# Kernel optimization log

Measured on AMD Instinct MI355X. Metric: run time of the kernel, lower is better.

## Reference

```python
import jax, jax.numpy as jnp
import numpy as np

B, G, D_EMB = 4096, 20000, 512
H_LOW, N_HIDDEN = 512, 1024
TOPK, T, FILM_W = 64, 0.1, 1.0
LN_EPS = 1e-5


def _layer_norm(x, gamma, beta):
    mu = jnp.mean(x, axis=-1, keepdims=True)
    var = jnp.mean(jnp.square(x - mu), axis=-1, keepdims=True)
    return (x - mu) * jax.lax.rsqrt(var + LN_EPS) * gamma + beta


def _l2norm(x, eps=1e-12):
    n = jnp.sqrt(jnp.sum(jnp.square(x), axis=-1, keepdims=True))
    return x / jnp.maximum(n, eps)


def setup_inputs() -> dict:
    key = jax.random.key(0)
    ks = jax.random.split(key, 8)
    s = 0.02
    return {
        "x": jax.random.normal(ks[0], (B, G), jnp.float32),
        "g": jax.random.normal(ks[1], (G, D_EMB), jnp.float32),
        "W_enc": jax.random.normal(ks[2], (H_LOW, G), jnp.float32) * s,
        "b_enc": jnp.zeros((H_LOW,), jnp.float32),
        "ln1_g": jnp.ones((H_LOW,), jnp.float32),
        "ln1_b": jnp.zeros((H_LOW,), jnp.float32),
        "W_ga": jax.random.normal(ks[3], (H_LOW, D_EMB), jnp.float32) * s,
        "W_gamma": jax.random.normal(ks[4], (H_LOW, H_LOW), jnp.float32) * s,
        "b_gamma": jnp.zeros((H_LOW,), jnp.float32),
        "W_beta": jax.random.normal(ks[5], (H_LOW, H_LOW), jnp.float32) * s,
        "b_beta": jnp.zeros((H_LOW,), jnp.float32),
        "W_exp": jax.random.normal(ks[6], (N_HIDDEN, H_LOW), jnp.float32) * s,
        "b_exp": jnp.zeros((N_HIDDEN,), jnp.float32),
        "ln2_g": jnp.ones((N_HIDDEN,), jnp.float32),
        "ln2_b": jnp.zeros((N_HIDDEN,), jnp.float32),
    }


def reference(x, g, W_enc, b_enc, ln1_g, ln1_b, W_ga, W_gamma, b_gamma,
              W_beta, b_beta, W_exp, b_exp, ln2_g, ln2_b):
    # x_encoder: Linear -> LayerNorm -> GELU (dropout = eval no-op)
    h = jnp.dot(x, W_enc.T) + b_enc                    # [B, H_LOW]
    h = jax.nn.gelu(_layer_norm(h, ln1_g, ln1_b), approximate=False)
    # gene adapter + cosine scores
    e = _l2norm(jnp.dot(g, W_ga.T))                    # [G, H_LOW]
    h_x = _l2norm(h)                                   # [B, H_LOW]
    scores = jnp.dot(h_x, e.T) / T                     # [B, G]
    # top-k mask + masked softmax attention
    _, idx = jax.lax.top_k(scores, TOPK)               # [B, TOPK]
    mask = jnp.zeros_like(scores).at[jnp.arange(B)[:, None], idx].set(1.0)
    attn = jax.nn.softmax(jnp.where(mask == 0, -1e9, scores), axis=-1)
    ctx = jnp.dot(attn, e)                             # [B, H_LOW]
    # FiLM (identity-centered)
    gamma = (jnp.dot(ctx, W_gamma.T) + b_gamma) * FILM_W
    beta = (jnp.dot(ctx, W_beta.T) + b_beta) * FILM_W
    h_cell = (1.0 + gamma) * h_x + beta
    # x_expand: Linear -> LayerNorm -> GELU
    h2 = jnp.dot(h_cell, W_exp.T) + b_exp              # [B, N_HIDDEN]
    return jax.nn.gelu(_layer_norm(h2, ln2_g, ln2_b), approximate=False)
```

## Files before the change

### kernel.cpp

```cpp
#include <hip/hip_runtime.h>
#include <hip/hip_fp16.h>
#include <math.h>
#include <type_traits>

#define DEVI __device__ __forceinline__

typedef __attribute__((ext_vector_type(8))) short bf16x8;
typedef __attribute__((ext_vector_type(4))) float f32x4;
typedef __attribute__((ext_vector_type(4))) unsigned int u32x4;
typedef unsigned short ushort_t;

DEVI unsigned int pack_bf16(float a, float b) {
  unsigned int ua = __float_as_uint(a), ub = __float_as_uint(b);
  ua = (ua + 0x7FFFu + ((ua >> 16) & 1u)) >> 16;
  ub = (ub + 0x7FFFu + ((ub >> 16) & 1u)) >> 16;
  return ua | (ub << 16);
}

DEVI bf16x8 cvt_bf16x8(f32x4 lo, f32x4 hi) {
  unsigned int r0, r1, r2, r3;
  asm("v_cvt_pk_bf16_f32 %0, %1, %2" : "=v"(r0) : "v"(lo[0]), "v"(lo[1]));
  asm("v_cvt_pk_bf16_f32 %0, %1, %2" : "=v"(r1) : "v"(lo[2]), "v"(lo[3]));
  asm("v_cvt_pk_bf16_f32 %0, %1, %2" : "=v"(r2) : "v"(hi[0]), "v"(hi[1]));
  asm("v_cvt_pk_bf16_f32 %0, %1, %2" : "=v"(r3) : "v"(hi[2]), "v"(hi[3]));
  union { u32x4 u; bf16x8 v; } x;
  x.u = u32x4{r0, r1, r2, r3};
  return x.v;
}

template<int SPLITZ, typename OutT>
__global__ __launch_bounds__(512, 1) void bgemm256(
    const ushort_t* __restrict__ A, const ushort_t* __restrict__ B,
    OutT* __restrict__ C, int M, int N, int K, int nbn, int nbm)
{
  __shared__ __align__(16) char L[131072];
  const int tid = threadIdx.x, lane = tid & 63, wv = tid >> 6;

  const int nwg = gridDim.x;
  const int hw = blockIdx.x;
  const int q = nwg >> 3, r = nwg & 7;
  const int xcd = hw & 7, pos = hw >> 3;
  const int lid = (xcd < r ? xcd * (q + 1) : r * (q + 1) + (xcd - r) * q) + pos;
  const int bn = lid % nbn;
  const int t2 = lid / nbn;
  const int bm = t2 % nbm;
  const int z  = t2 / nbm;

  const int ksteps = K >> 6;
  int kbBeg = 0, kbEnd = ksteps;
  if (SPLITZ > 1) {
    const int sz = (ksteps + SPLITZ - 1) / SPLITZ;
    kbBeg = z * sz;
    kbEnd = min(ksteps, kbBeg + sz);
  }

  const int wm = wv >> 2, wn = wv & 3;
  const int lrow = lane & 15, kg = lane >> 4;

  f32x4 acc[8][4];
#pragma unroll
  for (int i = 0; i < 8; ++i)
#pragma unroll
    for (int j = 0; j < 4; ++j) acc[i][j] = f32x4{0.f, 0.f, 0.f, 0.f};

  const int sr = lane >> 2, sq = lane & 3;
  const ushort_t* aS[2];
  const ushort_t* bS[2];
#pragma unroll
  for (int j = 0; j < 2; ++j) {
    const int lr = (wv * 2 + j) * 16 + sr;
    const int swz = (lr ^ (lr >> 2)) & 3;
    aS[j] = A + (size_t)min(bm * 256 + lr, M - 1) * (size_t)K + ((sq ^ swz) << 3);
    bS[j] = B + (size_t)min(bn * 256 + lr, N - 1) * (size_t)K + ((sq ^ swz) << 3);
  }

  int offA[8], offB[4];
#pragma unroll
  for (int i = 0; i < 8; ++i) {
    const int ra = wm * 128 + i * 16 + lrow;
    offA[i] = ra * 64 + (((kg ^ ((ra ^ (ra >> 2)) & 3))) << 4);
  }
#pragma unroll
  for (int j = 0; j < 4; ++j) {
    const int rb = wn * 64 + j * 16 + lrow;
    offB[j] = rb * 64 + (((kg ^ ((rb ^ (rb >> 2)) & 3))) << 4);
  }

#define G256_STG(isB, h, k0v) do {                                            \
    _Pragma("unroll")                                                         \
    for (int j_ = 0; j_ < 2; ++j_)                                            \
      __builtin_amdgcn_global_load_lds(                                       \
          (const __attribute__((address_space(1))) void*)                     \
              (((isB) ? bS : aS)[j_] + (k0v) + (h) * 32),                     \
          (__attribute__((address_space(3))) void*)                           \
              (L + (isB) * 65536 + (s ^ 1) * 32768 + (h) * 16384 +            \
               (wv * 2 + j_) * 1024), 16, 0, 0);                              \
  } while (0)
#define G256_RDA(h, rg) do {                                                  \
    _Pragma("unroll")                                                         \
    for (int i_ = 0; i_ < 4; ++i_)                                            \
      af[i_] = *(const bf16x8*)(L + s * 32768 + (h) * 16384 +                 \
                                offA[(rg) * 4 + i_]);                         \
  } while (0)
#define G256_RDB(h) do {                                                      \
    _Pragma("unroll")                                                         \
    for (int j_ = 0; j_ < 4; ++j_)                                            \
      bfv[j_] = *(const bf16x8*)(L + 65536 + s * 32768 + (h) * 16384 +        \
                                 offB[j_]);                                   \
  } while (0)
#define G256_MM(rg) do {                                                      \
    _Pragma("unroll")                                                         \
    for (int i_ = 0; i_ < 4; ++i_)                                            \
      _Pragma("unroll")                                                       \
      for (int j_ = 0; j_ < 4; ++j_)                                          \
        acc[(rg) * 4 + i_][j_] = __builtin_amdgcn_mfma_f32_16x16x32_bf16(     \
            af[i_], bfv[j_], acc[(rg) * 4 + i_][j_], 0, 0, 0);                \
  } while (0)
#define G256_BAR asm volatile("s_barrier" ::: "memory")

  {
    int s = 1;
    const int k0 = kbBeg << 6;
    G256_STG(0, 0, k0);
    G256_STG(1, 0, k0);
    G256_STG(0, 1, k0);
    G256_STG(1, 1, k0);
  }
  asm volatile("s_waitcnt vmcnt(4)" ::: "memory");
  G256_BAR;

  int s = 0;
  for (int t = kbBeg; t < kbEnd; ++t) {
    const bool more = (t + 1 < kbEnd);
    const int k0n = (t + 1) << 6;
    bf16x8 af[4], bfv[4];
    G256_RDB(0);
    G256_RDA(0, 0);
    if (more) G256_STG(0, 0, k0n);
    G256_BAR;
    __builtin_amdgcn_s_setprio(1);
    G256_MM(0);
    __builtin_amdgcn_s_setprio(0);
    G256_BAR;
    G256_RDA(0, 1);
    if (more) G256_STG(1, 0, k0n);
    G256_BAR;
    __builtin_amdgcn_s_setprio(1);
    G256_MM(1);
    __builtin_amdgcn_s_setprio(0);
    if (more) asm volatile("s_waitcnt vmcnt(4)" ::: "memory");
    else      asm volatile("s_waitcnt vmcnt(0)" ::: "memory");
    G256_BAR;
    G256_RDB(1);
    G256_RDA(1, 0);
    if (more) G256_STG(0, 1, k0n);
    G256_BAR;
    __builtin_amdgcn_s_setprio(1);
    G256_MM(0);
    __builtin_amdgcn_s_setprio(0);
    G256_BAR;
    G256_RDA(1, 1);
    if (more) G256_STG(1, 1, k0n);
    G256_BAR;
    __builtin_amdgcn_s_setprio(1);
    G256_MM(1);
    __builtin_amdgcn_s_setprio(0);
    if (more) asm volatile("s_waitcnt vmcnt(4)" ::: "memory");
    G256_BAR;
    s ^= 1;
  }
#undef G256_STG
#undef G256_RDA
#undef G256_RDB
#undef G256_MM
#undef G256_BAR

  const size_t zoff = (SPLITZ > 1) ? (size_t)z * (size_t)M * (size_t)N : 0;
#pragma unroll
  for (int i = 0; i < 8; ++i) {
#pragma unroll
    for (int j = 0; j < 4; ++j) {
      const int col = bn * 256 + wn * 64 + j * 16 + lrow;
      if (col >= N) continue;
      const int row0 = bm * 256 + wm * 128 + i * 16 + kg * 4;
#pragma unroll
      for (int rr = 0; rr < 4; ++rr) {
        const int gr = row0 + rr;
        if (gr < M) {
          const float v = acc[i][j][rr];
          if constexpr (std::is_same<OutT, __half>::value)
            C[zoff + (size_t)gr * (size_t)N + col] = __float2half(v);
          else
            C[zoff + (size_t)gr * (size_t)N + col] = v;
        }
      }
    }
  }
}

template<typename AT, int SPLITZ, bool DUALB, bool BIAS, typename OutT>
__global__ __launch_bounds__(512, sizeof(AT) == 2 ? 3 : 2) void bgemm(
    const AT* __restrict__ A, const ushort_t* __restrict__ B0,
    const ushort_t* __restrict__ B1, const float* __restrict__ bias0,
    const float* __restrict__ bias1, OutT* __restrict__ C,
    int M, int N, int K, int nbn, int nbm)
{
  constexpr bool AB16 = (sizeof(AT) == 2);
  __shared__ __align__(16) char AsB[AB16 ? 16384 : 32768];
  __shared__ __align__(16) char BsB[32768];
  const int tid = threadIdx.x, lane = tid & 63, wv = tid >> 6;

  const int nwg = gridDim.x;
  const int hw = blockIdx.x;
  const int q = nwg >> 3, r = nwg & 7;
  const int xcd = hw & 7, pos = hw >> 3;
  const int lid = (xcd < r ? xcd * (q + 1) : r * (q + 1) + (xcd - r) * q) + pos;
  const int bn = lid % nbn;
  const int t2 = lid / nbn;
  const int bm = t2 % nbm;
  const int z  = t2 / nbm;

  const ushort_t* B  = (DUALB && z == 1) ? B1 : B0;
  const float* bias  = (DUALB && z == 1) ? bias1 : bias0;

  const int ksteps = (K + 63) >> 6;
  int kbBeg = 0, kbEnd = ksteps;
  if (SPLITZ > 1) {
    const int sz = (ksteps + SPLITZ - 1) / SPLITZ;
    kbBeg = z * sz;
    kbEnd = min(ksteps, kbBeg + sz);
  }

  const int wr = (wv >> 2) * 64;
  const int wc = (wv & 3) * 64;
  const int lrow = lane & 15, kg = lane >> 4;

  f32x4 acc[4][4];
#pragma unroll
  for (int i = 0; i < 4; ++i)
#pragma unroll
    for (int j = 0; j < 4; ++j) acc[i][j] = f32x4{0.f, 0.f, 0.f, 0.f};

  const AT* aSrc[4];
  if constexpr (AB16) {
    const int r0 = lane >> 3;
    const int ce = ((lane & 7) ^ r0) << 3;
#pragma unroll
    for (int j = 0; j < 2; ++j) {
      const int row = wv * 16 + j * 8 + r0;
      aSrc[j] = A + (size_t)min(bm * 128 + row, M - 1) * (size_t)K + ce;
    }
  } else {
    const int r0 = lane >> 4;
#pragma unroll
    for (int j = 0; j < 4; ++j) {
      const int row = wv * 16 + j * 4 + r0;
      const int ca = ((lane & 15) << 2) ^ ((row & 7) << 3);
      aSrc[j] = A + (size_t)min(bm * 128 + row, M - 1) * (size_t)K + ca;
    }
  }
  const int rB0 = lane >> 3;
  const int colB = ((lane & 7) ^ rB0) << 3;
  const ushort_t* bSrc[4];
#pragma unroll
  for (int j = 0; j < 4; ++j) {
    const int row = wv * 32 + j * 8 + rB0;
    bSrc[j] = B + (size_t)min(bn * 256 + row, N - 1) * (size_t)K + colB;
  }

  for (int kb = kbBeg; kb < kbEnd; ++kb) {
    const int k0 = kb << 6;
    if constexpr (AB16) {
#pragma unroll
      for (int j = 0; j < 2; ++j)
        __builtin_amdgcn_global_load_lds(
            (const __attribute__((address_space(1))) void*)(aSrc[j] + k0),
            (__attribute__((address_space(3))) void*)(AsB + (wv * 2 + j) * 1024),
            16, 0, 0);
    } else {
#pragma unroll
      for (int j = 0; j < 4; ++j)
        __builtin_amdgcn_global_load_lds(
            (const __attribute__((address_space(1))) void*)(aSrc[j] + k0),
            (__attribute__((address_space(3))) void*)(AsB + (wv * 4 + j) * 1024),
            16, 0, 0);
    }
#pragma unroll
    for (int j = 0; j < 4; ++j)
      __builtin_amdgcn_global_load_lds(
          (const __attribute__((address_space(1))) void*)(bSrc[j] + k0),
          (__attribute__((address_space(3))) void*)(BsB + (wv * 4 + j) * 1024),
          16, 0, 0);
    __syncthreads();
#pragma unroll
    for (int kk = 0; kk < 2; ++kk) {
      bf16x8 af[4], bfr[4];
#pragma unroll
      for (int i = 0; i < 4; ++i) {
        const int ra = wr + i * 16 + lrow;
        if constexpr (AB16) {
          af[i] = *(const bf16x8*)(AsB + ra * 128 + ((((kk << 2) + kg) ^ (ra & 7)) << 4));
        } else {
          const char* pa = AsB + ra * 256 + ((kk * 128 + (kg << 5)) ^ ((ra & 7) << 5));
          af[i] = cvt_bf16x8(*(const f32x4*)pa, *(const f32x4*)(pa + 16));
        }
        const int rb = wc + i * 16 + lrow;
        bfr[i] = *(const bf16x8*)(BsB + rb * 128 + ((((kk << 2) + kg) ^ (rb & 7)) << 4));
      }
#pragma unroll
      for (int i = 0; i < 4; ++i)
#pragma unroll
        for (int j = 0; j < 4; ++j)
          acc[i][j] = __builtin_amdgcn_mfma_f32_16x16x32_bf16(af[i], bfr[j], acc[i][j], 0, 0, 0);
    }
    __syncthreads();
  }

  const size_t zoff = (SPLITZ > 1 || DUALB) ? (size_t)z * (size_t)M * (size_t)N : 0;
#pragma unroll
  for (int i = 0; i < 4; ++i) {
#pragma unroll
    for (int j = 0; j < 4; ++j) {
      const int col = bn * 256 + wc + j * 16 + lrow;
      if (col >= N) continue;
      const int row0 = bm * 128 + wr + i * 16 + kg * 4;
      float bv = 0.f;
      if (BIAS) bv = bias[col];
#pragma unroll
      for (int rr = 0; rr < 4; ++rr) {
        const int gr = row0 + rr;
        if (gr < M) {
          const float v = acc[i][j][rr] + bv;
          if constexpr (std::is_same<OutT, __half>::value)
            C[zoff + (size_t)gr * (size_t)N + col] = __float2half(v);
          else
            C[zoff + (size_t)gr * (size_t)N + col] = v;
        }
      }
    }
  }
}

__global__ __launch_bounds__(256) void f2b(
    const float4* __restrict__ in, u32x4* __restrict__ out, int n8)
{
  const int i = blockIdx.x * 256 + threadIdx.x;
  if (i < n8) {
    const float4 a = in[2 * i], b = in[2 * i + 1];
    u32x4 o = { pack_bf16(a.x, a.y), pack_bf16(a.z, a.w),
                pack_bf16(b.x, b.y), pack_bf16(b.z, b.w) };
    out[i] = o;
  }
}

template<int K0_8, int KP_8>
__global__ __launch_bounds__(256) void f2b_pad(
    const float* __restrict__ in, u32x4* __restrict__ out, int total)
{
  const int i = blockIdx.x * 256 + threadIdx.x;
  if (i >= total) return;
  const int row = i / KP_8, c8 = i % KP_8;
  u32x4 o = {0u, 0u, 0u, 0u};
  if (c8 < K0_8) {
    const float4* p = (const float4*)(in + (size_t)row * (K0_8 * 8) + c8 * 8);
    const float4 a = p[0], b = p[1];
    o = u32x4{ pack_bf16(a.x, a.y), pack_bf16(a.z, a.w),
               pack_bf16(b.x, b.y), pack_bf16(b.z, b.w) };
  }
  out[i] = o;
}

__global__ __launch_bounds__(256) void gee_fuse_ln1(
    const float* __restrict__ P, const float* __restrict__ b_enc,
    const float* __restrict__ g1, const float* __restrict__ b1,
    float* __restrict__ hx, unsigned int* __restrict__ hxb)
{
  const int row = blockIdx.x, tid = threadIdx.x;
  __shared__ float red[16];
  const size_t MN = (size_t)4096 * 512;
  const size_t o2 = (size_t)row * 256 + tid;
  float2 v = ((const float2*)b_enc)[tid];
#pragma unroll
  for (int qq = 0; qq < 8; ++qq) {
    const float2 p = ((const float2*)P)[qq * (MN / 2) + o2];
    v.x += p.x; v.y += p.y;
  }
  float a = v.x + v.y;
  float b = v.x * v.x + v.y * v.y;
#pragma unroll
  for (int o = 32; o > 0; o >>= 1) { a += __shfl_xor(a, o); b += __shfl_xor(b, o); }
  const int lane = tid & 63, wvi = tid >> 6;
  if (lane == 0) { red[wvi] = a; red[8 + wvi] = b; }
  __syncthreads();
  const float mu  = (red[0] + red[1] + red[2] + red[3]) * (1.f / 512.f);
  const float ex2 = (red[8] + red[9] + red[10] + red[11]) * (1.f / 512.f);
  const float inv = rsqrtf(ex2 - mu * mu + 1e-5f);
  const float2 gg = ((const float2*)g1)[tid];
  const float2 bb = ((const float2*)b1)[tid];
  const float y0 = (v.x - mu) * inv * gg.x + bb.x;
  const float y1 = (v.y - mu) * inv * gg.y + bb.y;
  const float t0 = 0.5f * y0 * (1.f + erff(y0 * 0.70710678118654752f));
  const float t1 = 0.5f * y1 * (1.f + erff(y1 * 0.70710678118654752f));
  float ss = t0 * t0 + t1 * t1;
  __syncthreads();
#pragma unroll
  for (int o = 32; o > 0; o >>= 1) ss += __shfl_xor(ss, o);
  if (lane == 0) red[wvi] = ss;
  __syncthreads();
  const float sc = 1.f / fmaxf(sqrtf(red[0] + red[1] + red[2] + red[3]), 1e-12f);
  const float h0 = t0 * sc, h1 = t1 * sc;
  ((float2*)hx)[o2] = make_float2(h0, h1);
  hxb[o2] = pack_bf16(h0, h1);
}

__global__ __launch_bounds__(256) void gee_l2rows(
    const __half2* __restrict__ ein, unsigned int* __restrict__ eb)
{
  const int row = blockIdx.x, tid = threadIdx.x;
  __shared__ float red[4];
  const __half2 h = ein[(size_t)row * 256 + tid];
  const float vx = __half2float(h.x), vy = __half2float(h.y);
  float ss = vx * vx + vy * vy;
#pragma unroll
  for (int o = 32; o > 0; o >>= 1) ss += __shfl_xor(ss, o);
  if ((tid & 63) == 0) red[tid >> 6] = ss;
  __syncthreads();
  const float sc = 1.f / fmaxf(sqrtf(red[0] + red[1] + red[2] + red[3]), 1e-12f);
  eb[(size_t)row * 256 + tid] = pack_bf16(vx * sc, vy * sc);
}

__global__ __launch_bounds__(256) void gee_topk(
    const __half* __restrict__ scores, int* __restrict__ oidx, float* __restrict__ ow)
{
  constexpr int G = 20000, GP = G / 2, CAP = 2048, TCAP = 160;
  const int row = blockIdx.x, tid = threadIdx.x;
  const int lane = tid & 63, wv = tid >> 6;
  __shared__ int hist[4][256];
  __shared__ int cnt_ge[256];
  __shared__ int wtop[4];
  __shared__ unsigned int comp[CAP];
  __shared__ int whist[4][16];
  __shared__ int sel[64];
  __shared__ int tie[TCAP];
  __shared__ int s_thr, s_above, s_cand, s_cnt, s_n1, s_n2;

  const unsigned int* srow32 =
      (const unsigned int*)((const ushort_t*)scores + (size_t)row * G);
  const ushort_t* srow16 = (const ushort_t*)srow32;

#pragma unroll
  for (int b = 0; b < 4; ++b) hist[b][tid] = 0;
  if (tid == 0) { s_cnt = 0; s_n1 = 0; s_n2 = 0; }
  __syncthreads();

  for (int j0 = 0; j0 < GP; j0 += 256) {
    const int j = j0 + tid;
    if (j < GP) {
      const unsigned int p = srow32[j];
      const unsigned int f = (((p >> 15) & 0x10001u) * 0x7FFFu) + 0x80008000u;
      const unsigned int k2 = p ^ f;
      atomicAdd(&hist[wv][(k2 >> 8) & 0xFFu], 1);
      atomicAdd(&hist[wv][k2 >> 24], 1);
    }
  }
  __syncthreads();
  cnt_ge[tid] = hist[0][tid] + hist[1][tid] + hist[2][tid] + hist[3][tid];
  __syncthreads();
  for (int off = 1; off < 256; off <<= 1) {
    const int add = (tid + off < 256) ? cnt_ge[tid + off] : 0;
    __syncthreads();
    cnt_ge[tid] += add;
    __syncthreads();
  }
  {
    const unsigned long long m = __ballot(cnt_ge[tid] >= 64);
    if (lane == 0) wtop[wv] = m ? (wv * 64 + 63 - __clzll(m)) : -1;
  }
  __syncthreads();
  if (tid == 0) {
    const int thrB = max(max(wtop[0], wtop[1]), max(wtop[2], wtop[3]));
    s_cand  = cnt_ge[thrB];
    s_above = (thrB == 255) ? 0 : cnt_ge[thrB + 1];
    s_thr   = thrB << 8;
  }
  __syncthreads();

  const bool useComp = (s_cand <= CAP);
  const unsigned int thrB = ((unsigned int)s_thr) >> 8;

  if (useComp) {
    for (int j0 = 0; j0 < GP; j0 += 256) {
      const int j = j0 + tid;
      if (j < GP) {
        const unsigned int p = srow32[j];
        const unsigned int f = (((p >> 15) & 0x10001u) * 0x7FFFu) + 0x80008000u;
        const unsigned int k2 = p ^ f;
        const unsigned int lo = k2 & 0xFFFFu, hi = k2 >> 16;
        if ((lo >> 8) >= thrB) {
          const int pos = atomicAdd(&s_cnt, 1);
          comp[pos] = (lo << 16) | (unsigned)(2 * j);
        }
        if ((hi >> 8) >= thrB) {
          const int pos = atomicAdd(&s_cnt, 1);
          comp[pos] = (hi << 16) | (unsigned)(2 * j + 1);
        }
      }
    }
  }
  __syncthreads();
  const int Nloop = useComp ? s_cnt : G;

  for (int pass = 2; pass < 4; ++pass) {
    const int shift = 12 - 4 * pass;
    const unsigned int thr = (unsigned int)s_thr;
    const unsigned int pfx = thr >> (shift + 4);
    int c[16];
#pragma unroll
    for (int b = 0; b < 16; ++b) c[b] = 0;
    for (int j0 = 0; j0 < Nloop; j0 += 256) {
      const int j = j0 + tid;
      const bool ok = j < Nloop;
      unsigned int key;
      if (useComp) {
        key = ok ? (comp[j] >> 16) : 0u;
      } else {
        const unsigned int raw = ok ? (unsigned int)srow16[j] : 0u;
        key = (raw & 0x8000u) ? (0xFFFFu & ~raw) : (raw | 0x8000u);
      }
      const unsigned int nb = (ok && (key >> (shift + 4)) == pfx) ? ((key >> shift) & 15u) : 0xFFu;
#pragma unroll
      for (int b = 0; b < 16; ++b) c[b] += __popcll(__ballot(nb == (unsigned)b));
    }
    if (lane == 0) {
#pragma unroll
      for (int b = 0; b < 16; ++b) whist[wv][b] = c[b];
    }
    __syncthreads();
    if (tid == 0) {
      int run = s_above;
      for (int vv = 15; vv >= 0; --vv) {
        const int c4 = whist[0][vv] + whist[1][vv] + whist[2][vv] + whist[3][vv];
        if (run + c4 >= 64) { s_thr |= vv << shift; break; }
        run += c4;
      }
      s_above = run;
    }
    __syncthreads();
  }

  const unsigned int kthr = (unsigned int)s_thr;
  for (int j0 = 0; j0 < Nloop; j0 += 256) {
    const int j = j0 + tid;
    if (j < Nloop) {
      unsigned int key, idx;
      if (useComp) {
        const unsigned int u = comp[j];
        key = u >> 16; idx = u & 0xFFFFu;
      } else {
        const unsigned int raw = (unsigned int)srow16[j];
        key = (raw & 0x8000u) ? (0xFFFFu & ~raw) : (raw | 0x8000u);
        idx = (unsigned)j;
      }
      if (key > kthr) {
        const int pos = atomicAdd(&s_n1, 1);
        sel[pos] = (int)idx;
      } else if (key == kthr) {
        const int pos = atomicAdd(&s_n2, 1);
        if (pos < TCAP) tie[pos] = (int)idx;
      }
    }
  }
  __syncthreads();
  if (tid == 0) {
    const int n1 = s_n1;
    const int n2 = min(s_n2, TCAP);
    const int need = 64 - n1;
    for (int rr = 0; rr < need; ++rr) {
      int best = 1 << 30, bj = 0;
      for (int j = 0; j < n2; ++j)
        if (tie[j] < best) { best = tie[j]; bj = j; }
      sel[n1 + rr] = best;
      tie[bj] = 1 << 30;
    }
  }
  __syncthreads();
  if (tid < 64) {
    const int idx = sel[tid];
    const float sv = __half2float(scores[(size_t)row * G + idx]) * 10.0f;
    float m = sv;
#pragma unroll
    for (int o = 32; o > 0; o >>= 1) m = fmaxf(m, __shfl_xor(m, o));
    const float w = __expf(sv - m);
    float d = w;
#pragma unroll
    for (int o = 32; o > 0; o >>= 1) d += __shfl_xor(d, o);
    oidx[(size_t)row * 64 + tid] = idx;
    ow[(size_t)row * 64 + tid] = w / d;
  }
}

__global__ __launch_bounds__(256) void gee_ctx(
    const int* __restrict__ idx, const float* __restrict__ w,
    const unsigned int* __restrict__ eb, unsigned int* __restrict__ ctxb)
{
  const int row = blockIdx.x, tid = threadIdx.x;
  __shared__ int sidx[64];
  __shared__ float sw[64];
  if (tid < 64) { sidx[tid] = idx[(size_t)row * 64 + tid]; sw[tid] = w[(size_t)row * 64 + tid]; }
  __syncthreads();
  float a0 = 0.f, a1 = 0.f;
#pragma unroll 4
  for (int k = 0; k < 64; ++k) {
    const unsigned int pk = eb[(size_t)sidx[k] * 256 + tid];
    const float wk = sw[k];
    a0 += wk * __uint_as_float(pk << 16);
    a1 += wk * __uint_as_float(pk & 0xFFFF0000u);
  }
  ctxb[(size_t)row * 256 + tid] = pack_bf16(a0, a1);
}

__global__ __launch_bounds__(256) void gee_film(
    const float2* __restrict__ gm, const float2* __restrict__ bt,
    const float2* __restrict__ hx, unsigned int* __restrict__ hcb, int n2)
{
  const int i = blockIdx.x * 256 + threadIdx.x;
  if (i < n2) {
    const float2 g = gm[i], b = bt[i], h = hx[i];
    hcb[i] = pack_bf16((1.f + g.x) * h.x + b.x, (1.f + g.y) * h.y + b.y);
  }
}

__global__ __launch_bounds__(256) void gee_ln2(
    const float* __restrict__ h2, const float* __restrict__ g2,
    const float* __restrict__ b2, float* __restrict__ out)
{
  const int row = blockIdx.x, tid = threadIdx.x;
  __shared__ float red[16];
  float v[4];
  float a = 0.f, b = 0.f;
#pragma unroll
  for (int e = 0; e < 4; ++e) {
    v[e] = h2[(size_t)row * 1024 + tid + e * 256];
    a += v[e]; b += v[e] * v[e];
  }
#pragma unroll
  for (int o = 32; o > 0; o >>= 1) { a += __shfl_xor(a, o); b += __shfl_xor(b, o); }
  const int lane = tid & 63, wvi = tid >> 6;
  if (lane == 0) { red[wvi] = a; red[8 + wvi] = b; }
  __syncthreads();
  const float mu  = (red[0] + red[1] + red[2] + red[3]) * (1.f / 1024.f);
  const float ex2 = (red[8] + red[9] + red[10] + red[11]) * (1.f / 1024.f);
  const float inv = rsqrtf(ex2 - mu * mu + 1e-5f);
#pragma unroll
  for (int e = 0; e < 4; ++e) {
    const int c = tid + e * 256;
    const float y = (v[e] - mu) * inv * g2[c] + b2[c];
    out[(size_t)row * 1024 + c] = 0.5f * y * (1.f + erff(y * 0.70710678118654752f));
  }
}

extern "C" void kernel_launch(void* const* d_in, const int* in_sizes, int n_in,
                              void* d_out, int out_size, void* d_ws, size_t ws_size,
                              hipStream_t stream)
{
  const float* x       = (const float*)d_in[0];
  const float* g       = (const float*)d_in[1];
  const float* W_enc   = (const float*)d_in[2];
  const float* b_enc   = (const float*)d_in[3];
  const float* ln1_g   = (const float*)d_in[4];
  const float* ln1_b   = (const float*)d_in[5];
  const float* W_ga    = (const float*)d_in[6];
  const float* W_gamma = (const float*)d_in[7];
  const float* b_gamma = (const float*)d_in[8];
  const float* W_beta  = (const float*)d_in[9];
  const float* b_beta  = (const float*)d_in[10];
  const float* W_exp   = (const float*)d_in[11];
  const float* b_exp   = (const float*)d_in[12];
  const float* ln2_g   = (const float*)d_in[13];
  const float* ln2_b   = (const float*)d_in[14];
  float* out = (float*)d_out;

  char* ws = (char*)d_ws;
  constexpr size_t OFF_XB     = 0;
  constexpr size_t OFF_SCORES = 0;
  constexpr size_t OFF_GA     = 0;
  constexpr size_t OFF_BE     = 8388608;
  constexpr size_t OFF_H2     = 16777216;
  constexpr size_t OFF_PART   = 164626432;
  constexpr size_t OFF_WENCB  = 231735296;
  constexpr size_t OFF_E      = 231735296;
  constexpr size_t OFF_EB     = 252313600;
  constexpr size_t OFF_HX     = 272793600;
  constexpr size_t OFF_HXB    = 281182208;
  constexpr size_t OFF_CTXB   = 285376512;
  constexpr size_t OFF_HCB    = 289570816;
  constexpr size_t OFF_WGAB   = 293765120;
  constexpr size_t OFF_WGMB   = 294289408;
  constexpr size_t OFF_WBTB   = 294813696;
  constexpr size_t OFF_WEXB   = 295337984;
  constexpr size_t OFF_TIDX   = 296386560;
  constexpr size_t OFF_TW     = 297435136;

  ushort_t*     xb     = (ushort_t*)(ws + OFF_XB);
  __half*       scores = (__half*)(ws + OFF_SCORES);
  float*        ga     = (float*)(ws + OFF_GA);
  float*        be     = (float*)(ws + OFF_BE);
  float*        h2     = (float*)(ws + OFF_H2);
  float*        part   = (float*)(ws + OFF_PART);
  ushort_t*     wencb  = (ushort_t*)(ws + OFF_WENCB);
  __half*       e      = (__half*)(ws + OFF_E);
  unsigned int* eb     = (unsigned int*)(ws + OFF_EB);
  float*        hx     = (float*)(ws + OFF_HX);
  unsigned int* hxb    = (unsigned int*)(ws + OFF_HXB);
  unsigned int* ctxb   = (unsigned int*)(ws + OFF_CTXB);
  unsigned int* hcb    = (unsigned int*)(ws + OFF_HCB);
  ushort_t*     wgab   = (ushort_t*)(ws + OFF_WGAB);
  ushort_t*     wgmb   = (ushort_t*)(ws + OFF_WGMB);
  ushort_t*     wbtb   = (ushort_t*)(ws + OFF_WBTB);
  ushort_t*     wexb   = (ushort_t*)(ws + OFF_WEXB);
  int*          tidx   = (int*)(ws + OFF_TIDX);
  float*        tw     = (float*)(ws + OFF_TW);

  f2b_pad<2500, 2512><<<40192, 256, 0, stream>>>(x, (u32x4*)xb, 4096 * 2512);
  f2b_pad<2500, 2512><<<5024, 256, 0, stream>>>(W_enc, (u32x4*)wencb, 512 * 2512);
  f2b<<<128, 256, 0, stream>>>((const float4*)W_ga,    (u32x4*)wgab, 32768);
  f2b<<<128, 256, 0, stream>>>((const float4*)W_gamma, (u32x4*)wgmb, 32768);
  f2b<<<128, 256, 0, stream>>>((const float4*)W_beta,  (u32x4*)wbtb, 32768);
  f2b<<<256, 256, 0, stream>>>((const float4*)W_exp,   (u32x4*)wexb, 65536);

  bgemm256<8, float><<<256, 512, 0, stream>>>(
      xb, wencb, part, 4096, 512, 20096, 2, 16);
  gee_fuse_ln1<<<4096, 256, 0, stream>>>(part, b_enc, ln1_g, ln1_b, hx, hxb);
  bgemm<float, 1, false, false, __half><<<314, 512, 0, stream>>>(
      g, wgab, nullptr, nullptr, nullptr, e, 20000, 512, 512, 2, 157);
  gee_l2rows<<<20000, 256, 0, stream>>>((const __half2*)e, eb);
  bgemm256<1, __half><<<1264, 512, 0, stream>>>(
      (const ushort_t*)hxb, (const ushort_t*)eb, scores, 4096, 20000, 512, 79, 16);
  gee_topk<<<4096, 256, 0, stream>>>(scores, tidx, tw);
  gee_ctx<<<4096, 256, 0, stream>>>(tidx, tw, eb, ctxb);
  bgemm<ushort_t, 1, true, true, float><<<128, 512, 0, stream>>>(
      (const ushort_t*)ctxb, wgmb, wbtb, b_gamma, b_beta, ga, 4096, 512, 512, 2, 32);
  gee_film<<<4096, 256, 0, stream>>>((const float2*)ga, (const float2*)be,
                                     (const float2*)hx, hcb, 1048576);
  bgemm<ushort_t, 1, false, true, float><<<128, 512, 0, stream>>>(
      (const ushort_t*)hcb, wexb, nullptr, b_exp, nullptr, h2, 4096, 1024, 512, 4, 32);
  gee_ln2<<<4096, 256, 0, stream>>>(h2, ln2_g, ln2_b, out);
}
```

Baseline: 561.5 us.

## Read fp32 x directly in encoder GEMM and fuse top-k with context gather

The explicit fp32-to-bf16 padded conversion of x (4096x20000) is replaced by a new GEMM that streams fp32 A tiles into LDS and converts them to bf16 in registers before the MFMA. This drops a full extra read and write of the large input, at the cost of doubled LDS/global traffic per A tile, a 128-row tile and a split-K of 4, plus a scalar tail for the unpadded K. Separately, the top-k kernel now performs the weighted context gather itself, which removes the index/weight round trip through global memory and one kernel launch.

```diff
diff --git a/kernel.cpp b/kernel.cpp
--- a/kernel.cpp
+++ b/kernel.cpp
@@ -26,6 +26,187 @@
   union { u32x4 u; bf16x8 v; } x;
   x.u = u32x4{r0, r1, r2, r3};
   return x.v;
+}
+
+template<int SPLITZ, bool TAIL>
+__global__ __launch_bounds__(512, 1) void bgemmA32(
+    const float* __restrict__ A, const ushort_t* __restrict__ B,
+    float* __restrict__ C, int M, int N, int K, int nbn, int nbm)
+{
+  __shared__ __align__(16) char L[131072];
+  const int tid = threadIdx.x, lane = tid & 63, wv = tid >> 6;
+
+  const int nwg = gridDim.x;
+  const int hw = blockIdx.x;
+  const int q = nwg >> 3, r = nwg & 7;
+  const int xcd = hw & 7, pos = hw >> 3;
+  const int lid = (xcd < r ? xcd * (q + 1) : r * (q + 1) + (xcd - r) * q) + pos;
+  const int bn = lid % nbn;
+  const int t2 = lid / nbn;
+  const int bm = t2 % nbm;
+  const int z  = t2 / nbm;
+
+  const int ksteps = K >> 6;
+  const int szk = (ksteps + SPLITZ - 1) / SPLITZ;
+  const int kbBeg = z * szk;
+  const int kbEnd = min(ksteps, kbBeg + szk);
+
+  const int wm = wv >> 2, wn = wv & 3;
+  const int lrow = lane & 15, kg = lane >> 4;
+
+  f32x4 acc[4][4];
+#pragma unroll
+  for (int i = 0; i < 4; ++i)
+#pragma unroll
+    for (int j = 0; j < 4; ++j) acc[i][j] = f32x4{0.f, 0.f, 0.f, 0.f};
+
+  const int alr = lane >> 3, ag32 = (lane & 7) >> 1;
+  const float* aS[2];
+#pragma unroll
+  for (int j = 0; j < 2; ++j) {
+    const int lr = (wv * 2 + j) * 8 + alr;
+    const int swz = (lr ^ (lr >> 2)) & 3;
+    const int colf = ((ag32 ^ swz) << 3) + (lane & 1) * 4;
+    aS[j] = A + (size_t)min(bm * 128 + lr, M - 1) * (size_t)K + colf;
+  }
+  const int blr = lane >> 2, bgq = lane & 3;
+  const ushort_t* bS[2];
+#pragma unroll
+  for (int j = 0; j < 2; ++j) {
+    const int lr = (wv * 2 + j) * 16 + blr;
+    const int swz = (lr ^ (lr >> 2)) & 3;
+    aS[j] = aS[j];
+    bS[j] = B + (size_t)min(bn * 256 + lr, N - 1) * (size_t)K + ((bgq ^ swz) << 3);
+  }
+
+  int offA[4], offB[4];
+#pragma unroll
+  for (int i = 0; i < 4; ++i) {
+    const int ra = wm * 64 + i * 16 + lrow;
+    offA[i] = ra * 128 + ((kg ^ ((ra ^ (ra >> 2)) & 3)) << 5);
+  }
+#pragma unroll
+  for (int j = 0; j < 4; ++j) {
+    const int rb = wn * 64 + j * 16 + lrow;
+    offB[j] = rb * 64 + ((kg ^ ((rb ^ (rb >> 2)) & 3)) << 4);
+  }
+
+#define GA_STGA(h, k0v) do {                                                  \
+    _Pragma("unroll")                                                         \
+    for (int j_ = 0; j_ < 2; ++j_)                                            \
+      __builtin_amdgcn_global_load_lds(                                       \
+          (const __attribute__((address_space(1))) void*)(aS[j_] + (k0v) + (h) * 32), \
+          (__attribute__((address_space(3))) void*)                           \
+              (L + (s ^ 1) * 32768 + (h) * 16384 + (wv * 2 + j_) * 1024),     \
+          16, 0, 0);                                                          \
+  } while (0)
+#define GA_STGB(h, k0v) do {                                                  \
+    _Pragma("unroll")                                                         \
+    for (int j_ = 0; j_ < 2; ++j_)                                            \
+      __builtin_amdgcn_global_load_lds(                                       \
+          (const __attribute__((address_space(1))) void*)(bS[j_] + (k0v) + (h) * 32), \
+          (__attribute__((address_space(3))) void*)                           \
+              (L + 65536 + (s ^ 1) * 32768 + (h) * 16384 + (wv * 2 + j_) * 1024), \
+          16, 0, 0);                                                          \
+  } while (0)
+#define GA_RDB(h) do {                                                        \
+    _Pragma("unroll")                                                         \
+    for (int j_ = 0; j_ < 4; ++j_)                                            \
+      bfv[j_] = *(const bf16x8*)(L + 65536 + s * 32768 + (h) * 16384 + offB[j_]); \
+  } while (0)
+#define GA_RDA(h, rg) do {                                                    \
+    _Pragma("unroll")                                                         \
+    for (int i_ = 0; i_ < 2; ++i_) {                                          \
+      const char* pa_ = L + s * 32768 + (h) * 16384 + offA[(rg) * 2 + i_];    \
+      af[i_] = cvt_bf16x8(*(const f32x4*)pa_, *(const f32x4*)(pa_ + 16));     \
+    }                                                                         \
+  } while (0)
+#define GA_MM(rg) do {                                                        \
+    _Pragma("unroll")                                                         \
+    for (int i_ = 0; i_ < 2; ++i_)                                            \
+      _Pragma("unroll")                                                       \
+      for (int j_ = 0; j_ < 4; ++j_)                                          \
+        acc[(rg) * 2 + i_][j_] = __builtin_amdgcn_mfma_f32_16x16x32_bf16(     \
+            af[i_], bfv[j_], acc[(rg) * 2 + i_][j_], 0, 0, 0);                \
+  } while (0)
+#define GA_BAR asm volatile("s_barrier" ::: "memory")
+
+  {
+    int s = 1;
+    const int k0 = kbBeg << 6;
+    GA_STGA(0, k0); GA_STGB(0, k0); GA_STGA(1, k0); GA_STGB(1, k0);
+  }
+  asm volatile("s_waitcnt vmcnt(4)" ::: "memory");
+  GA_BAR;
+
+  int s = 0;
+  for (int t = kbBeg; t < kbEnd; ++t) {
+    const bool more = (t + 1 < kbEnd);
+    const int k0n = (t + 1) << 6;
+    bf16x8 af[2], bfv[4];
+    GA_RDB(0); GA_RDA(0, 0);
+    if (more) GA_STGA(0, k0n);
+    GA_BAR;
+    __builtin_amdgcn_s_setprio(1); GA_MM(0); __builtin_amdgcn_s_setprio(0);
+    GA_BAR;
+    GA_RDA(0, 1);
+    if (more) GA_STGB(0, k0n);
+    GA_BAR;
+    __builtin_amdgcn_s_setprio(1); GA_MM(1); __builtin_amdgcn_s_setprio(0);
+    if (more) asm volatile("s_waitcnt vmcnt(4)" ::: "memory");
+    else      asm volatile("s_waitcnt vmcnt(0)" ::: "memory");
+    GA_BAR;
+    GA_RDB(1); GA_RDA(1, 0);
+    if (more) GA_STGA(1, k0n);
+    GA_BAR;
+    __builtin_amdgcn_s_setprio(1); GA_MM(0); __builtin_amdgcn_s_setprio(0);
+    GA_BAR;
+    GA_RDA(1, 1);
+    if (more) GA_STGB(1, k0n);
+    GA_BAR;
+    __builtin_amdgcn_s_setprio(1); GA_MM(1); __builtin_amdgcn_s_setprio(0);
+    if (more) asm volatile("s_waitcnt vmcnt(4)" ::: "memory");
+    GA_BAR;
+    s ^= 1;
+  }
+
+  if (TAIL && z == SPLITZ - 1 && (K & 63)) {
+    const int k0t = ksteps << 6;
+    bf16x8 af[2], bfv[4];
+#pragma unroll
+    for (int j = 0; j < 2; ++j) {
+      const float4 av = *(const float4*)(aS[j] + k0t);
+      *(float4*)(L + s * 32768 + (wv * 2 + j) * 1024 + lane * 16) = av;
+      const u32x4 bv = *(const u32x4*)(bS[j] + k0t);
+      *(u32x4*)(L + 65536 + s * 32768 + (wv * 2 + j) * 1024 + lane * 16) = bv;
+    }
+    __syncthreads();
+    GA_RDB(0);
+    GA_RDA(0, 0); GA_MM(0);
+    GA_RDA(0, 1); GA_MM(1);
+  }
+#undef GA_STGA
+#undef GA_STGB
+#undef GA_RDB
+#undef GA_RDA
+#undef GA_MM
+#undef GA_BAR
+
+  const size_t zoff = (SPLITZ > 1) ? (size_t)z * (size_t)M * (size_t)N : 0;
+#pragma unroll
+  for (int i = 0; i < 4; ++i) {
+#pragma unroll
+    for (int j = 0; j < 4; ++j) {
+      const int col = bn * 256 + wn * 64 + j * 16 + lrow;
+      if (col >= N) continue;
+      const int row0 = bm * 128 + wm * 64 + i * 16 + kg * 4;
+#pragma unroll
+      for (int rr = 0; rr < 4; ++rr) {
+        const int gr = row0 + rr;
+        if (gr < M) C[zoff + (size_t)gr * (size_t)N + col] = acc[i][j][rr];
+      }
+    }
+  }
 }
 
 template<int SPLITZ, typename OutT>
@@ -138,16 +319,12 @@
     G256_RDA(0, 0);
     if (more) G256_STG(0, 0, k0n);
     G256_BAR;
-    __builtin_amdgcn_s_setprio(1);
-    G256_MM(0);
-    __builtin_amdgcn_s_setprio(0);
+    __builtin_amdgcn_s_setprio(1); G256_MM(0); __builtin_amdgcn_s_setprio(0);
     G256_BAR;
     G256_RDA(0, 1);
     if (more) G256_STG(1, 0, k0n);
     G256_BAR;
-    __builtin_amdgcn_s_setprio(1);
-    G256_MM(1);
-    __builtin_amdgcn_s_setprio(0);
+    __builtin_amdgcn_s_setprio(1); G256_MM(1); __builtin_amdgcn_s_setprio(0);
     if (more) asm volatile("s_waitcnt vmcnt(4)" ::: "memory");
     else      asm volatile("s_waitcnt vmcnt(0)" ::: "memory");
     G256_BAR;
@@ -155,16 +332,12 @@
     G256_RDA(1, 0);
     if (more) G256_STG(0, 1, k0n);
     G256_BAR;
-    __builtin_amdgcn_s_setprio(1);
-    G256_MM(0);
-    __builtin_amdgcn_s_setprio(0);
+    __builtin_amdgcn_s_setprio(1); G256_MM(0); __builtin_amdgcn_s_setprio(0);
     G256_BAR;
     G256_RDA(1, 1);
     if (more) G256_STG(1, 1, k0n);
     G256_BAR;
-    __builtin_amdgcn_s_setprio(1);
-    G256_MM(1);
-    __builtin_amdgcn_s_setprio(0);
+    __builtin_amdgcn_s_setprio(1); G256_MM(1); __builtin_amdgcn_s_setprio(0);
     if (more) asm volatile("s_waitcnt vmcnt(4)" ::: "memory");
     G256_BAR;
     s ^= 1;
@@ -353,23 +526,6 @@
   }
 }
 
-template<int K0_8, int KP_8>
-__global__ __launch_bounds__(256) void f2b_pad(
-    const float* __restrict__ in, u32x4* __restrict__ out, int total)
-{
-  const int i = blockIdx.x * 256 + threadIdx.x;
-  if (i >= total) return;
-  const int row = i / KP_8, c8 = i % KP_8;
-  u32x4 o = {0u, 0u, 0u, 0u};
-  if (c8 < K0_8) {
-    const float4* p = (const float4*)(in + (size_t)row * (K0_8 * 8) + c8 * 8);
-    const float4 a = p[0], b = p[1];
-    o = u32x4{ pack_bf16(a.x, a.y), pack_bf16(a.z, a.w),
-               pack_bf16(b.x, b.y), pack_bf16(b.z, b.w) };
-  }
-  out[i] = o;
-}
-
 __global__ __launch_bounds__(256) void gee_fuse_ln1(
     const float* __restrict__ P, const float* __restrict__ b_enc,
     const float* __restrict__ g1, const float* __restrict__ b1,
@@ -381,7 +537,7 @@
   const size_t o2 = (size_t)row * 256 + tid;
   float2 v = ((const float2*)b_enc)[tid];
 #pragma unroll
-  for (int qq = 0; qq < 8; ++qq) {
+  for (int qq = 0; qq < 4; ++qq) {
     const float2 p = ((const float2*)P)[qq * (MN / 2) + o2];
     v.x += p.x; v.y += p.y;
   }
@@ -429,8 +585,9 @@
   eb[(size_t)row * 256 + tid] = pack_bf16(vx * sc, vy * sc);
 }
 
-__global__ __launch_bounds__(256) void gee_topk(
-    const __half* __restrict__ scores, int* __restrict__ oidx, float* __restrict__ ow)
+__global__ __launch_bounds__(256) void gee_topk_ctx(
+    const __half* __restrict__ scores, const unsigned int* __restrict__ eb,
+    unsigned int* __restrict__ ctxb)
 {
   constexpr int G = 20000, GP = G / 2, CAP = 2048, TCAP = 160;
   const int row = blockIdx.x, tid = threadIdx.x;
@@ -441,6 +598,7 @@
   __shared__ unsigned int comp[CAP];
   __shared__ int whist[4][16];
   __shared__ int sel[64];
+  __shared__ float swt[64];
   __shared__ int tie[TCAP];
   __shared__ int s_thr, s_above, s_cand, s_cnt, s_n1, s_n2;
 
@@ -594,25 +752,14 @@
     float d = w;
 #pragma unroll
     for (int o = 32; o > 0; o >>= 1) d += __shfl_xor(d, o);
-    oidx[(size_t)row * 64 + tid] = idx;
-    ow[(size_t)row * 64 + tid] = w / d;
-  }
-}
-
-__global__ __launch_bounds__(256) void gee_ctx(
-    const int* __restrict__ idx, const float* __restrict__ w,
-    const unsigned int* __restrict__ eb, unsigned int* __restrict__ ctxb)
-{
-  const int row = blockIdx.x, tid = threadIdx.x;
-  __shared__ int sidx[64];
-  __shared__ float sw[64];
-  if (tid < 64) { sidx[tid] = idx[(size_t)row * 64 + tid]; sw[tid] = w[(size_t)row * 64 + tid]; }
+    swt[tid] = w / d;
+  }
   __syncthreads();
   float a0 = 0.f, a1 = 0.f;
 #pragma unroll 4
   for (int k = 0; k < 64; ++k) {
-    const unsigned int pk = eb[(size_t)sidx[k] * 256 + tid];
-    const float wk = sw[k];
+    const unsigned int pk = eb[(size_t)sel[k] * 256 + tid];
+    const float wk = swt[k];
     a0 += wk * __uint_as_float(pk << 16);
     a1 += wk * __uint_as_float(pk & 0xFFFF0000u);
   }
@@ -681,27 +828,23 @@
   float* out = (float*)d_out;
 
   char* ws = (char*)d_ws;
-  constexpr size_t OFF_XB     = 0;
   constexpr size_t OFF_SCORES = 0;
   constexpr size_t OFF_GA     = 0;
   constexpr size_t OFF_BE     = 8388608;
   constexpr size_t OFF_H2     = 16777216;
-  constexpr size_t OFF_PART   = 164626432;
-  constexpr size_t OFF_WENCB  = 231735296;
-  constexpr size_t OFF_E      = 231735296;
-  constexpr size_t OFF_EB     = 252313600;
-  constexpr size_t OFF_HX     = 272793600;
-  constexpr size_t OFF_HXB    = 281182208;
-  constexpr size_t OFF_CTXB   = 285376512;
-  constexpr size_t OFF_HCB    = 289570816;
-  constexpr size_t OFF_WGAB   = 293765120;
-  constexpr size_t OFF_WGMB   = 294289408;
-  constexpr size_t OFF_WBTB   = 294813696;
-  constexpr size_t OFF_WEXB   = 295337984;
-  constexpr size_t OFF_TIDX   = 296386560;
-  constexpr size_t OFF_TW     = 297435136;
-
-  ushort_t*     xb     = (ushort_t*)(ws + OFF_XB);
+  constexpr size_t OFF_PART   = 163840000;
+  constexpr size_t OFF_WENCB  = 197394432;
+  constexpr size_t OFF_E      = 197394432;
+  constexpr size_t OFF_EB     = 217874432;
+  constexpr size_t OFF_HX     = 238354432;
+  constexpr size_t OFF_HXB    = 246743040;
+  constexpr size_t OFF_CTXB   = 250937344;
+  constexpr size_t OFF_HCB    = 255131648;
+  constexpr size_t OFF_WGAB   = 259325952;
+  constexpr size_t OFF_WGMB   = 259850240;
+  constexpr size_t OFF_WBTB   = 260374528;
+  constexpr size_t OFF_WEXB   = 260898816;
+
   __half*       scores = (__half*)(ws + OFF_SCORES);
   float*        ga     = (float*)(ws + OFF_GA);
   float*        be     = (float*)(ws + OFF_BE);
@@ -718,26 +861,22 @@
   ushort_t*     wgmb   = (ushort_t*)(ws + OFF_WGMB);
   ushort_t*     wbtb   = (ushort_t*)(ws + OFF_WBTB);
   ushort_t*     wexb   = (ushort_t*)(ws + OFF_WEXB);
-  int*          tidx   = (int*)(ws + OFF_TIDX);
-  float*        tw     = (float*)(ws + OFF_TW);
-
-  f2b_pad<2500, 2512><<<40192, 256, 0, stream>>>(x, (u32x4*)xb, 4096 * 2512);
-  f2b_pad<2500, 2512><<<5024, 256, 0, stream>>>(W_enc, (u32x4*)wencb, 512 * 2512);
-  f2b<<<128, 256, 0, stream>>>((const float4*)W_ga,    (u32x4*)wgab, 32768);
-  f2b<<<128, 256, 0, stream>>>((const float4*)W_gamma, (u32x4*)wgmb, 32768);
-  f2b<<<128, 256, 0, stream>>>((const float4*)W_beta,  (u32x4*)wbtb, 32768);
-  f2b<<<256, 256, 0, stream>>>((const float4*)W_exp,   (u32x4*)wexb, 65536);
-
-  bgemm256<8, float><<<256, 512, 0, stream>>>(
-      xb, wencb, part, 4096, 512, 20096, 2, 16);
+
+  f2b<<<5000, 256, 0, stream>>>((const float4*)W_enc,   (u32x4*)wencb, 1280000);
+  f2b<<<128,  256, 0, stream>>>((const float4*)W_ga,    (u32x4*)wgab,  32768);
+  f2b<<<128,  256, 0, stream>>>((const float4*)W_gamma, (u32x4*)wgmb,  32768);
+  f2b<<<128,  256, 0, stream>>>((const float4*)W_beta,  (u32x4*)wbtb,  32768);
+  f2b<<<256,  256, 0, stream>>>((const float4*)W_exp,   (u32x4*)wexb,  65536);
+
+  bgemmA32<4, true><<<256, 512, 0, stream>>>(
+      x, wencb, part, 4096, 512, 20000, 2, 32);
   gee_fuse_ln1<<<4096, 256, 0, stream>>>(part, b_enc, ln1_g, ln1_b, hx, hxb);
   bgemm<float, 1, false, false, __half><<<314, 512, 0, stream>>>(
       g, wgab, nullptr, nullptr, nullptr, e, 20000, 512, 512, 2, 157);
   gee_l2rows<<<20000, 256, 0, stream>>>((const __half2*)e, eb);
   bgemm256<1, __half><<<1264, 512, 0, stream>>>(
       (const ushort_t*)hxb, (const ushort_t*)eb, scores, 4096, 20000, 512, 79, 16);
-  gee_topk<<<4096, 256, 0, stream>>>(scores, tidx, tw);
-  gee_ctx<<<4096, 256, 0, stream>>>(tidx, tw, eb, ctxb);
+  gee_topk_ctx<<<4096, 256, 0, stream>>>(scores, eb, ctxb);
   bgemm<ushort_t, 1, true, true, float><<<128, 512, 0, stream>>>(
       (const ushort_t*)ctxb, wgmb, wbtb, b_gamma, b_beta, ga, 4096, 512, 512, 2, 32);
   gee_film<<<4096, 256, 0, stream>>>((const float2*)ga, (const float2*)be,
```

New measurement: 503.9 us. 10.3% less time.
